# Performance work log

Hardware: AMD Instinct MI355X
Metric: run time of the kernel (lower is better)

Reference implementation:

```python
import jax, jax.numpy as jnp
import numpy as np

B, L, D, H, HD = 4, 4096, 512, 8, 64
BS = 64                 # block_size
NB = L // BS            # num blocks (== max_num_blocks)
MAXNB = 64


def setup_inputs() -> dict:
    key = jax.random.key(0)
    ks = jax.random.split(key, 11)
    s_in = 1.0 / np.sqrt(D)
    s_hd = 1.0 / np.sqrt(HD)
    s_o = 1.0 / np.sqrt(H * HD)
    return {
        "inputs_q": jax.random.normal(ks[0], (B, L, D), jnp.float32),
        "Wq": jax.random.normal(ks[1], (D, H, HD), jnp.float32) * s_in,
        "bq": jnp.zeros((H, HD), jnp.float32),
        "Wk": jax.random.normal(ks[2], (D, H, HD), jnp.float32) * s_in,
        "bk": jnp.zeros((H, HD), jnp.float32),
        "Wv": jax.random.normal(ks[3], (D, H, HD), jnp.float32) * s_in,
        "bv": jnp.zeros((H, HD), jnp.float32),
        "Wsort": jax.random.normal(ks[4], (HD, MAXNB), jnp.float32) * s_hd,
        "bsort": jnp.zeros((MAXNB,), jnp.float32),
        "Wout": jax.random.normal(ks[5], (H, HD, D), jnp.float32) * s_o,
        "bout": jnp.zeros((D,), jnp.float32),
    }


def _block_attention(q, k, v):
    # q,k,v: [b, n_blocks, block, heads, head_dim]; attention within each block
    scale = 1.0 / np.sqrt(HD)
    scores = jnp.einsum("bnqhd,bnkhd->bnhqk", q, k) * scale
    w = jax.nn.softmax(scores, axis=-1)
    return jnp.einsum("bnhqk,bnkhd->bnqhd", w, v)


def reference(inputs_q, Wq, bq, Wk, bk, Wv, bv, Wsort, bsort, Wout, bout):
    # self-attention: inputs_kv = inputs_q; seq_len == blocks_total_len so no padding
    q = jnp.einsum("bld,dhk->blhk", inputs_q, Wq) + bq
    k = jnp.einsum("bld,dhk->blhk", inputs_q, Wk) + bk
    v = jnp.einsum("bld,dhk->blhk", inputs_q, Wv) + bv

    block_q = q.reshape(B, NB, BS, H, HD)
    block_k = k.reshape(B, NB, BS, H, HD)
    block_v = v.reshape(B, NB, BS, H, HD)

    # non-causal: sum keys within each block -> [b, n_kv, h, hd]
    sum_key = jnp.sum(block_k, axis=2)
    sort_out = jnp.einsum("bnhk,ko->bnho", sum_key, Wsort) + bsort
    sort_out = sort_out[:, :, :, :NB]
    permutation = jax.nn.softmax(sort_out, axis=-1)  # [b, n_kv, h, n_q]

    # faithful to original einsum subscripts ('k' and 'l' both contracted)
    sorted_key = jnp.einsum("bkshd,bnhl->bnshd", block_k, permutation)
    sorted_value = jnp.einsum("bkshd,bnhl->bnshd", block_v, permutation)

    x = _block_attention(block_q, block_k, block_v)
    x = x + _block_attention(block_q, sorted_key, sorted_value)

    x = x.reshape(B, L, H, HD)
    out = jnp.einsum("blhd,hdf->blf", x, Wout) + bout
    return out
```

## Files before the change

kernel.cpp:

```cpp
#include <hip/hip_runtime.h>


constexpr int BB   = 4;
constexpr int LL   = 4096;
constexpr int DD   = 512;
constexpr int HH   = 8;
constexpr int HDIM = 64;
constexpr int BS   = 64;
constexpr int NBLK = 64;
constexpr int MTOT = BB * LL;

using f32x4  = __attribute__((ext_vector_type(4))) float;
typedef __attribute__((ext_vector_type(8))) __bf16 bf16x8;

static __device__ __forceinline__ ushort f2bf(float f) {
  uint u = __float_as_uint(f);
  uint r = (u + 0x7fffu + ((u >> 16) & 1u)) >> 16;
  return (ushort)r;
}
static __device__ __forceinline__ float bf2f(ushort u) { return __uint_as_float((uint)u << 16); }
static __device__ __forceinline__ float bflo(uint u) { return __uint_as_float(u << 16); }
static __device__ __forceinline__ float bfhi(uint u) { return __uint_as_float(u & 0xffff0000u); }

static __device__ __forceinline__ int swb(int row, int cb) {
  return (row << 6) + ((cb ^ ((row & 7) << 4)) >> 1);
}

#define GLOBAL_AS(p) ((const __attribute__((address_space(1))) void*)(p))
#define LDS_AS(p)    ((__attribute__((address_space(3))) void*)(p))
#define SB0()        __builtin_amdgcn_sched_barrier(0)

__global__ __launch_bounds__(256) void f32_to_bf16_vec(
    const float* __restrict__ src, ushort* __restrict__ dst)
{
  const int i = blockIdx.x * 256 + threadIdx.x;
  float4 v = reinterpret_cast<const float4*>(src)[i];
  ushort4 o;
  o.x = f2bf(v.x); o.y = f2bf(v.y); o.z = f2bf(v.z); o.w = f2bf(v.w);
  reinterpret_cast<ushort4*>(dst)[i] = o;
}

__global__ __launch_bounds__(256) void transpose_cast4(
    const float* __restrict__ Wq, const float* __restrict__ Wk,
    const float* __restrict__ Wv, const float* __restrict__ Wo,
    ushort* __restrict__ Wqkv_t, ushort* __restrict__ Wout_t)
{
  __shared__ float tile[32][33];
  const int z  = blockIdx.z;
  const float* src = (z == 0) ? Wq : (z == 1) ? Wk : (z == 2) ? Wv : Wo;
  ushort* dst = (z < 3) ? (Wqkv_t + (size_t)z * 512 * 512) : Wout_t;
  const int tx = threadIdx.x & 31, ty = threadIdx.x >> 5;
  const int r0 = blockIdx.y * 32, c0 = blockIdx.x * 32;
  #pragma unroll
  for (int q = 0; q < 4; ++q)
    tile[ty + 8 * q][tx] = src[(size_t)(r0 + ty + 8 * q) * 512 + c0 + tx];
  __syncthreads();
  #pragma unroll
  for (int q = 0; q < 4; ++q)
    dst[(size_t)(c0 + ty + 8 * q) * 512 + r0 + tx] = f2bf(tile[tx][ty + 8 * q]);
}

template<int MODE>
__global__ __launch_bounds__(256, 3) void gemm_pipe3(
    const ushort* __restrict__ A, const ushort* __restrict__ Bt,
    const float* __restrict__ b0, const float* __restrict__ b1,
    const float* __restrict__ b2,
    ushort* __restrict__ Cq, ushort* __restrict__ Ck, ushort* __restrict__ Cv,
    float* __restrict__ Cf, int N, int NBX)
{
  constexpr int K  = 512;
  constexpr int NT = K / 32;
  constexpr int TN = 128;
  __shared__ __align__(16) ushort sA[3][128 * 32];
  __shared__ __align__(16) ushort sB[3][128 * 32];

  const int tid  = threadIdx.x;
  const int lane = tid & 63;
  const int w    = tid >> 6;
  const int wr   = w >> 1, wc = w & 1;
  const int lr   = lane & 15;
  const int kq   = lane >> 4;

  const int nwg  = NBX * 128;
  const int cpx  = nwg >> 3;
  const int swz  = ((int)blockIdx.x & 7) * cpx + ((int)blockIdx.x >> 3);
  const int nb   = swz % NBX;
  const int mb   = swz / NBX;
  const int brow = mb * 128;
  const int bcol = nb * TN;

  auto stageA = [&](int buf, int t, int j) {
    const int c   = j * 256 + tid;
    const int row = c >> 2, ch = c & 3;
    const ushort* src = A + (size_t)(brow + row) * K + t * 32 + ((ch ^ ((row >> 1) & 3)) << 3);
    __builtin_amdgcn_global_load_lds(GLOBAL_AS(src),
        LDS_AS(&sA[buf][(j * 256 + (w << 6)) << 3]), 16, 0, 0);
  };
  auto stageB = [&](int buf, int t, int j) {
    const int c   = j * 256 + tid;
    const int row = c >> 2, ch = c & 3;
    const ushort* src = Bt + (size_t)(bcol + row) * K + t * 32 + ((ch ^ ((row >> 1) & 3)) << 3);
    __builtin_amdgcn_global_load_lds(GLOBAL_AS(src),
        LDS_AS(&sB[buf][(j * 256 + (w << 6)) << 3]), 16, 0, 0);
  };
  auto ldA = [&](int buf, int mf) -> bf16x8 {
    const int row = (wr << 6) + (mf << 4) + lr;
    return *reinterpret_cast<const bf16x8*>(&sA[buf][(row << 5) + ((kq ^ ((row >> 1) & 3)) << 3)]);
  };
  auto ldB = [&](int buf, int nf) -> bf16x8 {
    const int row = (wc << 6) + (nf << 4) + lr;
    return *reinterpret_cast<const bf16x8*>(&sB[buf][(row << 5) + ((kq ^ ((row >> 1) & 3)) << 3)]);
  };

  f32x4 acc[4][4];
  #pragma unroll
  for (int mi = 0; mi < 4; ++mi)
    #pragma unroll
    for (int ni = 0; ni < 4; ++ni)
      acc[mi][ni] = (f32x4){0.f, 0.f, 0.f, 0.f};

  stageA(0, 0, 0); stageA(0, 0, 1); stageB(0, 0, 0); stageB(0, 0, 1);
  stageA(1, 1, 0); stageA(1, 1, 1); stageB(1, 1, 0); stageB(1, 1, 1);
  asm volatile("s_waitcnt vmcnt(4)" ::: "memory");
  SB0(); __builtin_amdgcn_s_barrier(); SB0();

  for (int t = 0; t < NT; ++t) {
    const int buf  = t % 3;
    const int nbuf = (t + 2) % 3;
    const bool more = (t + 2) < NT;

    bf16x8 af[4], bfr[4];
    #pragma unroll
    for (int mf = 0; mf < 4; ++mf) af[mf] = ldA(buf, mf);
    #pragma unroll
    for (int nf = 0; nf < 4; ++nf) bfr[nf] = ldB(buf, nf);
    if (more) { stageA(nbuf, t + 2, 0); stageA(nbuf, t + 2, 1);
                stageB(nbuf, t + 2, 0); stageB(nbuf, t + 2, 1); }
    SB0();
    __builtin_amdgcn_s_setprio(1);
    #pragma unroll
    for (int mi = 0; mi < 4; ++mi)
      #pragma unroll
      for (int ni = 0; ni < 4; ++ni)
        acc[mi][ni] = __builtin_amdgcn_mfma_f32_16x16x32_bf16(af[mi], bfr[ni], acc[mi][ni], 0, 0, 0);
    __builtin_amdgcn_s_setprio(0);
    SB0();
    if (more) asm volatile("s_waitcnt vmcnt(4)" ::: "memory");
    else      asm volatile("s_waitcnt vmcnt(0)" ::: "memory");
    SB0(); __builtin_amdgcn_s_barrier(); SB0();
  }

  if constexpr (MODE == 0) {
    ushort* sEp = (ushort*)&sA[0][0];
    constexpr int ES = TN + 16;
    const int which = bcol >> 9;
    ushort* dst = (which == 0) ? Cq : ((which == 1) ? Ck : Cv);
    const float* bsel = (which == 0) ? b0 : ((which == 1) ? b1 : b2);
    const int ncol0 = bcol & 511;
    #pragma unroll
    for (int mi = 0; mi < 4; ++mi) {
      if (mi) __syncthreads();
      #pragma unroll
      for (int nf = 0; nf < 4; ++nf) {
        const int col = wc * 64 + nf * 16 + lr;
        const float bb = bsel[ncol0 + col];
        #pragma unroll
        for (int r = 0; r < 4; ++r)
          sEp[(wr * 16 + kq * 4 + r) * ES + col] = f2bf(acc[mi][nf][r] + bb);
      }
      __syncthreads();
      #pragma unroll
      for (int it = 0; it < 2; ++it) {
        const int idx = tid + it * 256;
        const int rr  = idx >> 4;
        const int cc  = (idx & 15) * 8;
        uint4 v = *reinterpret_cast<const uint4*>(&sEp[rr * ES + cc]);
        const int grow = brow + (rr >> 4) * 64 + mi * 16 + (rr & 15);
        *reinterpret_cast<uint4*>(&dst[(size_t)grow * DD + ncol0 + cc]) = v;
      }
    }
  } else {
    float* sEpF = (float*)&sA[0][0];
    constexpr int ES = TN + 8;
    #pragma unroll
    for (int mi = 0; mi < 4; ++mi) {
      if (mi) __syncthreads();
      #pragma unroll
      for (int nf = 0; nf < 4; ++nf) {
        const int col = wc * 64 + nf * 16 + lr;
        const float bb = b0[bcol + col];
        #pragma unroll
        for (int r = 0; r < 4; ++r)
          sEpF[(wr * 16 + kq * 4 + r) * ES + col] = acc[mi][nf][r] + bb;
      }
      __syncthreads();
      #pragma unroll
      for (int it = 0; it < 4; ++it) {
        const int idx = tid + it * 256;
        const int rr  = idx >> 5;
        const int cc  = (idx & 31) * 4;
        float4 v = *reinterpret_cast<const float4*>(&sEpF[rr * ES + cc]);
        const int grow = brow + (rr >> 4) * 64 + mi * 16 + (rr & 15);
        *reinterpret_cast<float4*>(&Cf[(size_t)grow * N + bcol + cc]) = v;
      }
    }
  }
}

__global__ __launch_bounds__(256) void sumkv_fused(
    const ushort* __restrict__ K, const ushort* __restrict__ V,
    ushort* __restrict__ Khi, ushort* __restrict__ Klo, ushort* __restrict__ Vb)
{
  __shared__ float kbuf[4][64][9];
  __shared__ float vbuf[4][64][9];
  const int bs   = blockIdx.x;
  const int b    = bs >> 6, s = bs & 63;
  const int lane = threadIdx.x & 63;
  const int kbq  = threadIdx.x >> 6;
  const size_t rowbase = ((size_t)b * LL + s) * DD + lane * 8;

  uint4 ku[16], vu[16];
  #pragma unroll
  for (int i = 0; i < 16; ++i) {
    const size_t off = rowbase + (size_t)(kbq * 16 + i) * BS * DD;
    ku[i] = *reinterpret_cast<const uint4*>(K + off);
    vu[i] = *reinterpret_cast<const uint4*>(V + off);
  }
  float ak[8] = {0,0,0,0,0,0,0,0}, av[8] = {0,0,0,0,0,0,0,0};
  #pragma unroll
  for (int i = 0; i < 16; ++i) {
    ak[0] += bflo(ku[i].x); ak[1] += bfhi(ku[i].x); ak[2] += bflo(ku[i].y); ak[3] += bfhi(ku[i].y);
    ak[4] += bflo(ku[i].z); ak[5] += bfhi(ku[i].z); ak[6] += bflo(ku[i].w); ak[7] += bfhi(ku[i].w);
    av[0] += bflo(vu[i].x); av[1] += bfhi(vu[i].x); av[2] += bflo(vu[i].y); av[3] += bfhi(vu[i].y);
    av[4] += bflo(vu[i].z); av[5] += bfhi(vu[i].z); av[6] += bflo(vu[i].w); av[7] += bfhi(vu[i].w);
  }
  #pragma unroll
  for (int j = 0; j < 8; ++j) { kbuf[kbq][lane][j] = ak[j]; vbuf[kbq][lane][j] = av[j]; }
  __syncthreads();

  const size_t wbase = (size_t)bs * DD + lane * 8;
  if (kbq == 0) {
    uint4 hi4, lo4;
    uint* hp = reinterpret_cast<uint*>(&hi4);
    uint* lp = reinterpret_cast<uint*>(&lo4);
    #pragma unroll
    for (int p = 0; p < 4; ++p) {
      uint hw = 0, lw = 0;
      #pragma unroll
      for (int q = 0; q < 2; ++q) {
        const int j = p * 2 + q;
        const float t = kbuf[0][lane][j] + kbuf[1][lane][j] +
                        kbuf[2][lane][j] + kbuf[3][lane][j];
        const ushort h = f2bf(t);
        const ushort l = f2bf(t - bf2f(h));
        hw |= (uint)h << (16 * q);
        lw |= (uint)l << (16 * q);
      }
      hp[p] = hw; lp[p] = lw;
    }
    *reinterpret_cast<uint4*>(Khi + wbase) = hi4;
    *reinterpret_cast<uint4*>(Klo + wbase) = lo4;
  } else if (kbq == 1) {
    uint4 o4;
    uint* op = reinterpret_cast<uint*>(&o4);
    #pragma unroll
    for (int p = 0; p < 4; ++p) {
      uint wv = 0;
      #pragma unroll
      for (int q = 0; q < 2; ++q) {
        const int j = p * 2 + q;
        const float t = vbuf[0][lane][j] + vbuf[1][lane][j] +
                        vbuf[2][lane][j] + vbuf[3][lane][j];
        wv |= (uint)f2bf(t) << (16 * q);
      }
      op[p] = wv;
    }
    *reinterpret_cast<uint4*>(Vb + wbase) = o4;
  }
}

__global__ __launch_bounds__(256) void attn_mfma(
    const ushort* __restrict__ Q, const ushort* __restrict__ Kg,
    const ushort* __restrict__ Vg, const ushort* __restrict__ Khi,
    const ushort* __restrict__ Klo, const ushort* __restrict__ Vsb,
    ushort* __restrict__ X)
{
  __shared__ __align__(16) ushort sA[64 * 64];
  __shared__ __align__(16) ushort sVt[64 * 64];
  __shared__ __align__(16) ushort sCP[64 * 64];
  const int bid = blockIdx.x;
  const int swz = (bid & 7) * 256 + (bid >> 3);
  const int n = swz & 63, h = (swz >> 6) & 7, b = swz >> 9;
  const int tid  = threadIdx.x;
  const int lane = tid & 63;
  const int w    = tid >> 6;
  const int lr   = lane & 15, hi4 = lane >> 4;
  const float scale = 0.125f;

  const size_t tbase = ((size_t)(b * LL + n * BS)) * DD + h * HDIM;
  const size_t sbase = ((size_t)(b * BS)) * DD + h * HDIM;

  uint4 k1[2], v1[2], k2h[2], k2l[2], v2[2];
  int rr[2], cc[2];
  #pragma unroll
  for (int it = 0; it < 2; ++it) {
    const int i  = tid + it * 256;
    const int r  = i >> 3;
    const int c8 = (i & 7) << 3;
    rr[it] = r; cc[it] = c8;
    const size_t g1 = tbase + (size_t)r * DD + c8;
    const size_t g2 = sbase + (size_t)r * DD + c8;
    k1[it]  = *reinterpret_cast<const uint4*>(Kg  + g1);
    v1[it]  = *reinterpret_cast<const uint4*>(Vg  + g1);
    k2h[it] = *reinterpret_cast<const uint4*>(Khi + g2);
    k2l[it] = *reinterpret_cast<const uint4*>(Klo + g2);
    v2[it]  = *reinterpret_cast<const uint4*>(Vsb + g2);
  }
  bf16x8 qf[2];
  #pragma unroll
  for (int ks = 0; ks < 2; ++ks)
    qf[ks] = *reinterpret_cast<const bf16x8*>(
        Q + tbase + (size_t)(w * 16 + lr) * DD + ks * 32 + hi4 * 8);

  #pragma unroll
  for (int it = 0; it < 2; ++it) {
    *reinterpret_cast<uint4*>(&sA[swb(rr[it], cc[it] << 1)]) = k1[it];
    const uint u[4] = {v1[it].x, v1[it].y, v1[it].z, v1[it].w};
    #pragma unroll
    for (int j = 0; j < 4; ++j) {
      sVt[swb(cc[it] + 2 * j,     rr[it] << 1)] = (ushort)(u[j] & 0xffff);
      sVt[swb(cc[it] + 2 * j + 1, rr[it] << 1)] = (ushort)(u[j] >> 16);
    }
  }
  __syncthreads();

  f32x4 xacc[4];
  #pragma unroll
  for (int dt = 0; dt < 4; ++dt) xacc[dt] = (f32x4){0.f, 0.f, 0.f, 0.f};

  {
    f32x4 st[4];
    #pragma unroll
    for (int t = 0; t < 4; ++t) st[t] = (f32x4){0.f, 0.f, 0.f, 0.f};
    #pragma unroll
    for (int ks = 0; ks < 2; ++ks) {
      #pragma unroll
      for (int t = 0; t < 4; ++t) {
        bf16x8 kf = *reinterpret_cast<const bf16x8*>(
            &sA[swb(t * 16 + lr, (ks * 32 + hi4 * 8) << 1)]);
        st[t] = __builtin_amdgcn_mfma_f32_16x16x32_bf16(kf, qf[ks], st[t], 0, 0, 0);
      }
    }
    float e[4][4];
    float mx = -1e30f;
    #pragma unroll
    for (int t = 0; t < 4; ++t)
      #pragma unroll
      for (int r = 0; r < 4; ++r) { e[t][r] = st[t][r] * scale; mx = fmaxf(mx, e[t][r]); }
    mx = fmaxf(mx, __shfl_xor(mx, 16));
    mx = fmaxf(mx, __shfl_xor(mx, 32));
    float sum = 0.f;
    #pragma unroll
    for (int t = 0; t < 4; ++t)
      #pragma unroll
      for (int r = 0; r < 4; ++r) { e[t][r] = __expf(e[t][r] - mx); sum += e[t][r]; }
    sum += __shfl_xor(sum, 16);
    sum += __shfl_xor(sum, 32);
    const float inv = 1.0f / sum;
    #pragma unroll
    for (int t = 0; t < 4; ++t) {
      ushort4 p4;
      p4.x = f2bf(e[t][0] * inv); p4.y = f2bf(e[t][1] * inv);
      p4.z = f2bf(e[t][2] * inv); p4.w = f2bf(e[t][3] * inv);
      *reinterpret_cast<ushort4*>(&sCP[swb(w * 16 + lr, (t * 16 + hi4 * 4) << 1)]) = p4;
    }
    #pragma unroll
    for (int ks = 0; ks < 2; ++ks) {
      bf16x8 pa = *reinterpret_cast<const bf16x8*>(
          &sCP[swb(w * 16 + lr, (ks * 32 + hi4 * 8) << 1)]);
      #pragma unroll
      for (int dt = 0; dt < 4; ++dt) {
        bf16x8 vb = *reinterpret_cast<const bf16x8*>(
            &sVt[swb(dt * 16 + lr, (ks * 32 + hi4 * 8) << 1)]);
        xacc[dt] = __builtin_amdgcn_mfma_f32_16x16x32_bf16(pa, vb, xacc[dt], 0, 0, 0);
      }
    }
  }
  __syncthreads();

  #pragma unroll
  for (int it = 0; it < 2; ++it) {
    *reinterpret_cast<uint4*>(&sA[swb(rr[it], cc[it] << 1)])  = k2h[it];
    *reinterpret_cast<uint4*>(&sCP[swb(rr[it], cc[it] << 1)]) = k2l[it];
    const uint u[4] = {v2[it].x, v2[it].y, v2[it].z, v2[it].w};
    #pragma unroll
    for (int j = 0; j < 4; ++j) {
      sVt[swb(cc[it] + 2 * j,     rr[it] << 1)] = (ushort)(u[j] & 0xffff);
      sVt[swb(cc[it] + 2 * j + 1, rr[it] << 1)] = (ushort)(u[j] >> 16);
    }
  }
  __syncthreads();

  {
    f32x4 st[4];
    #pragma unroll
    for (int t = 0; t < 4; ++t) st[t] = (f32x4){0.f, 0.f, 0.f, 0.f};
    #pragma unroll
    for (int ks = 0; ks < 2; ++ks) {
      #pragma unroll
      for (int t = 0; t < 4; ++t) {
        bf16x8 kh = *reinterpret_cast<const bf16x8*>(
            &sA[swb(t * 16 + lr, (ks * 32 + hi4 * 8) << 1)]);
        st[t] = __builtin_amdgcn_mfma_f32_16x16x32_bf16(kh, qf[ks], st[t], 0, 0, 0);
        bf16x8 kl = *reinterpret_cast<const bf16x8*>(
            &sCP[swb(t * 16 + lr, (ks * 32 + hi4 * 8) << 1)]);
        st[t] = __builtin_amdgcn_mfma_f32_16x16x32_bf16(kl, qf[ks], st[t], 0, 0, 0);
      }
    }
    __syncthreads();
    float e[4][4];
    float mx = -1e30f;
    #pragma unroll
    for (int t = 0; t < 4; ++t)
      #pragma unroll
      for (int r = 0; r < 4; ++r) { e[t][r] = st[t][r] * scale; mx = fmaxf(mx, e[t][r]); }
    mx = fmaxf(mx, __shfl_xor(mx, 16));
    mx = fmaxf(mx, __shfl_xor(mx, 32));
    float sum = 0.f;
    #pragma unroll
    for (int t = 0; t < 4; ++t)
      #pragma unroll
      for (int r = 0; r < 4; ++r) { e[t][r] = __expf(e[t][r] - mx); sum += e[t][r]; }
    sum += __shfl_xor(sum, 16);
    sum += __shfl_xor(sum, 32);
    const float inv = 1.0f / sum;
    #pragma unroll
    for (int t = 0; t < 4; ++t) {
      ushort4 p4;
      p4.x = f2bf(e[t][0] * inv); p4.y = f2bf(e[t][1] * inv);
      p4.z = f2bf(e[t][2] * inv); p4.w = f2bf(e[t][3] * inv);
      *reinterpret_cast<ushort4*>(&sCP[swb(w * 16 + lr, (t * 16 + hi4 * 4) << 1)]) = p4;
    }
    #pragma unroll
    for (int ks = 0; ks < 2; ++ks) {
      bf16x8 pa = *reinterpret_cast<const bf16x8*>(
          &sCP[swb(w * 16 + lr, (ks * 32 + hi4 * 8) << 1)]);
      #pragma unroll
      for (int dt = 0; dt < 4; ++dt) {
        bf16x8 vb = *reinterpret_cast<const bf16x8*>(
            &sVt[swb(dt * 16 + lr, (ks * 32 + hi4 * 8) << 1)]);
        xacc[dt] = __builtin_amdgcn_mfma_f32_16x16x32_bf16(pa, vb, xacc[dt], 0, 0, 0);
      }
    }
  }

  #pragma unroll
  for (int dt = 0; dt < 4; ++dt)
    #pragma unroll
    for (int r = 0; r < 4; ++r)
      X[tbase + (size_t)(w * 16 + hi4 * 4 + r) * DD + dt * 16 + lr] = f2bf(xacc[dt][r]);
}

extern "C" void kernel_launch(void* const* d_in, const int* in_sizes, int n_in,
                              void* d_out, int out_size, void* d_ws, size_t ws_size,
                              hipStream_t stream) {
  const float* x_in = (const float*)d_in[0];
  const float* Wq   = (const float*)d_in[1];
  const float* bq   = (const float*)d_in[2];
  const float* Wk   = (const float*)d_in[3];
  const float* bk   = (const float*)d_in[4];
  const float* Wv   = (const float*)d_in[5];
  const float* bv   = (const float*)d_in[6];
  const float* Wout = (const float*)d_in[9];
  const float* bout = (const float*)d_in[10];
  float* out = (float*)d_out;

  const size_t NTOK = (size_t)MTOT * DD;
  const size_t NSUM = (size_t)BB * BS * DD;
  char* ws = (char*)d_ws;
  ushort* xb      = (ushort*)ws;            ws += NTOK * 2;
  ushort* Qb      = (ushort*)ws;            ws += NTOK * 2;
  ushort* Kb      = (ushort*)ws;            ws += NTOK * 2;
  ushort* Vb      = (ushort*)ws;            ws += NTOK * 2;
  ushort* Xb      = (ushort*)ws;            ws += NTOK * 2;
  ushort* Wqkv_t  = (ushort*)ws;            ws += (size_t)1536 * 512 * 2;
  ushort* Wout_t  = (ushort*)ws;            ws += (size_t)512 * 512 * 2;
  ushort* KhiB    = (ushort*)ws;            ws += NSUM * 2;
  ushort* KloB    = (ushort*)ws;            ws += NSUM * 2;
  ushort* VsB     = (ushort*)ws;            ws += NSUM * 2;

  f32_to_bf16_vec<<<NTOK / 4 / 256, 256, 0, stream>>>(x_in, xb);
  transpose_cast4<<<dim3(16, 16, 4), 256, 0, stream>>>(
      Wq, Wk, Wv, Wout, Wqkv_t, Wout_t);

  gemm_pipe3<0><<<12 * 128, 256, 0, stream>>>(
      xb, Wqkv_t, bq, bk, bv, Qb, Kb, Vb, nullptr, 1536, 12);

  sumkv_fused<<<BB * BS, 256, 0, stream>>>(Kb, Vb, KhiB, KloB, VsB);

  attn_mfma<<<BB * HH * NBLK, 256, 0, stream>>>(Qb, Kb, Vb, KhiB, KloB, VsB, Xb);

  gemm_pipe3<1><<<4 * 128, 256, 0, stream>>>(
      Xb, Wout_t, bout, nullptr, nullptr, nullptr, nullptr, nullptr, out, 512, 4);
}
```

Before: 99.69 us.

## Replace QKV GEMM with 256x128-tile, 512-thread, double-buffered four-phase kernel

The QKV projection moves from the shared three-stage 128x128 GEMM template to a dedicated kernel with 256x128 tiles, 8 waves, K-steps of 64 and double buffering. Each K-step is split into four barrier-separated MFMA phases, with next-tile global-to-LDS loads issued inside the first two. The larger tile is meant to raise operand reuse and cut the workgroup count. The cost is one workgroup per CU (launch bounds 512,1), more barriers per K-step and bigger LDS use. The output GEMM is split into its own non-templated kernel with unchanged logic.

```diff
diff --git a/kernel.cpp b/kernel.cpp
--- a/kernel.cpp
+++ b/kernel.cpp
@@ -60,17 +60,167 @@
     dst[(size_t)(c0 + ty + 8 * q) * 512 + r0 + tx] = f2bf(tile[tx][ty + 8 * q]);
 }
 
-template<int MODE>
-__global__ __launch_bounds__(256, 3) void gemm_pipe3(
+__global__ __launch_bounds__(512, 1) void qkv_4phase(
     const ushort* __restrict__ A, const ushort* __restrict__ Bt,
     const float* __restrict__ b0, const float* __restrict__ b1,
     const float* __restrict__ b2,
-    ushort* __restrict__ Cq, ushort* __restrict__ Ck, ushort* __restrict__ Cv,
-    float* __restrict__ Cf, int N, int NBX)
+    ushort* __restrict__ Cq, ushort* __restrict__ Ck, ushort* __restrict__ Cv)
+{
+  constexpr int K = 512;
+  __shared__ __align__(16) ushort sA[2][256 * 64];
+  __shared__ __align__(16) ushort sB[2][128 * 64];
+
+  const int tid  = threadIdx.x;
+  const int lane = tid & 63;
+  const int w    = tid >> 6;
+  const int wr   = w >> 1;
+  const int wc   = w & 1;
+  const int lr   = lane & 15;
+  const int kq   = lane >> 4;
+
+  const int cpx  = 768 >> 3;
+  const int swz  = ((int)blockIdx.x & 7) * cpx + ((int)blockIdx.x >> 3);
+  const int nb   = swz % 12;
+  const int mb   = swz / 12;
+  const int brow = mb * 256;
+  const int bcol = nb * 128;
+
+  auto stA = [&](int buf, int kt, int j) {
+    const int c = j * 512 + tid;
+    const int row = c >> 3, g = c & 7;
+    const ushort* src = A + (size_t)(brow + row) * K + kt * 64 + ((g ^ (row & 7)) << 3);
+    __builtin_amdgcn_global_load_lds(GLOBAL_AS(src),
+        LDS_AS(&sA[buf][(j * 512 + w * 64) * 8]), 16, 0, 0);
+  };
+  auto stB = [&](int buf, int kt, int j) {
+    const int c = j * 512 + tid;
+    const int row = c >> 3, g = c & 7;
+    const ushort* src = Bt + (size_t)(bcol + row) * K + kt * 64 + ((g ^ (row & 7)) << 3);
+    __builtin_amdgcn_global_load_lds(GLOBAL_AS(src),
+        LDS_AS(&sB[buf][(j * 512 + w * 64) * 8]), 16, 0, 0);
+  };
+  auto rdA = [&](int buf, int mf, int ks) -> bf16x8 {
+    const int row = wr * 64 + mf * 16 + lr;
+    return *reinterpret_cast<const bf16x8*>(
+        &sA[buf][(row << 6) + ((((ks << 2) + kq) ^ (row & 7)) << 3)]);
+  };
+  auto rdB = [&](int buf, int nf, int ks) -> bf16x8 {
+    const int row = wc * 64 + nf * 16 + lr;
+    return *reinterpret_cast<const bf16x8*>(
+        &sB[buf][(row << 6) + ((((ks << 2) + kq) ^ (row & 7)) << 3)]);
+  };
+
+  f32x4 acc[4][4];
+  #pragma unroll
+  for (int mf = 0; mf < 4; ++mf)
+    #pragma unroll
+    for (int nf = 0; nf < 4; ++nf)
+      acc[mf][nf] = (f32x4){0.f, 0.f, 0.f, 0.f};
+
+  stA(0, 0, 0); stA(0, 0, 1); stA(0, 0, 2); stA(0, 0, 3);
+  stB(0, 0, 0); stB(0, 0, 1);
+  asm volatile("s_waitcnt vmcnt(0)" ::: "memory");
+  SB0(); __builtin_amdgcn_s_barrier(); SB0();
+
+  #pragma unroll 1
+  for (int t = 0; t < 8; ++t) {
+    const int buf  = t & 1;
+    const int nbuf = buf ^ 1;
+    const bool st  = (t + 1) < 8;
+    bf16x8 br[4];
+
+    #pragma unroll
+    for (int nf = 0; nf < 4; ++nf) br[nf] = rdB(buf, nf, 0);
+    {
+      bf16x8 a0 = rdA(buf, 0, 0), a1 = rdA(buf, 1, 0);
+      if (st) { stA(nbuf, t + 1, 0); stA(nbuf, t + 1, 1); stB(nbuf, t + 1, 0); }
+      SB0(); __builtin_amdgcn_s_barrier(); SB0();
+      __builtin_amdgcn_s_setprio(1);
+      #pragma unroll
+      for (int nf = 0; nf < 4; ++nf) {
+        acc[0][nf] = __builtin_amdgcn_mfma_f32_16x16x32_bf16(a0, br[nf], acc[0][nf], 0, 0, 0);
+        acc[1][nf] = __builtin_amdgcn_mfma_f32_16x16x32_bf16(a1, br[nf], acc[1][nf], 0, 0, 0);
+      }
+      __builtin_amdgcn_s_setprio(0);
+    }
+    {
+      bf16x8 a2 = rdA(buf, 2, 0), a3 = rdA(buf, 3, 0);
+      if (st) { stA(nbuf, t + 1, 2); stA(nbuf, t + 1, 3); stB(nbuf, t + 1, 1); }
+      SB0(); __builtin_amdgcn_s_barrier(); SB0();
+      __builtin_amdgcn_s_setprio(1);
+      #pragma unroll
+      for (int nf = 0; nf < 4; ++nf) {
+        acc[2][nf] = __builtin_amdgcn_mfma_f32_16x16x32_bf16(a2, br[nf], acc[2][nf], 0, 0, 0);
+        acc[3][nf] = __builtin_amdgcn_mfma_f32_16x16x32_bf16(a3, br[nf], acc[3][nf], 0, 0, 0);
+      }
+      __builtin_amdgcn_s_setprio(0);
+    }
+    #pragma unroll
+    for (int nf = 0; nf < 4; ++nf) br[nf] = rdB(buf, nf, 1);
+    {
+      bf16x8 a0 = rdA(buf, 0, 1), a1 = rdA(buf, 1, 1);
+      SB0(); __builtin_amdgcn_s_barrier(); SB0();
+      __builtin_amdgcn_s_setprio(1);
+      #pragma unroll
+      for (int nf = 0; nf < 4; ++nf) {
+        acc[0][nf] = __builtin_amdgcn_mfma_f32_16x16x32_bf16(a0, br[nf], acc[0][nf], 0, 0, 0);
+        acc[1][nf] = __builtin_amdgcn_mfma_f32_16x16x32_bf16(a1, br[nf], acc[1][nf], 0, 0, 0);
+      }
+      __builtin_amdgcn_s_setprio(0);
+    }
+    {
+      bf16x8 a2 = rdA(buf, 2, 1), a3 = rdA(buf, 3, 1);
+      SB0(); __builtin_amdgcn_s_barrier(); SB0();
+      __builtin_amdgcn_s_setprio(1);
+      #pragma unroll
+      for (int nf = 0; nf < 4; ++nf) {
+        acc[2][nf] = __builtin_amdgcn_mfma_f32_16x16x32_bf16(a2, br[nf], acc[2][nf], 0, 0, 0);
+        acc[3][nf] = __builtin_amdgcn_mfma_f32_16x16x32_bf16(a3, br[nf], acc[3][nf], 0, 0, 0);
+      }
+      __builtin_amdgcn_s_setprio(0);
+      SB0();
+      if (st) asm volatile("s_waitcnt vmcnt(0)" ::: "memory");
+      SB0(); __builtin_amdgcn_s_barrier(); SB0();
+    }
+  }
+
+  ushort* sEp = (ushort*)&sA[0][0];
+  constexpr int ES = 128 + 16;
+  const int which = bcol >> 9;
+  ushort* dst = (which == 0) ? Cq : ((which == 1) ? Ck : Cv);
+  const float* bsel = (which == 0) ? b0 : ((which == 1) ? b1 : b2);
+  const int ncol0 = bcol & 511;
+  #pragma unroll
+  for (int mf = 0; mf < 4; ++mf) {
+    if (mf) __syncthreads();
+    #pragma unroll
+    for (int nf = 0; nf < 4; ++nf) {
+      const int col = wc * 64 + nf * 16 + lr;
+      const float bb = bsel[ncol0 + col];
+      #pragma unroll
+      for (int r = 0; r < 4; ++r)
+        sEp[(wr * 16 + kq * 4 + r) * ES + col] = f2bf(acc[mf][nf][r] + bb);
+    }
+    __syncthreads();
+    #pragma unroll
+    for (int it = 0; it < 2; ++it) {
+      const int idx = tid + it * 512;
+      const int rr  = idx >> 4;
+      const int cc  = (idx & 15) * 8;
+      uint4 v = *reinterpret_cast<const uint4*>(&sEp[rr * ES + cc]);
+      const int grow = brow + (rr >> 4) * 64 + mf * 16 + (rr & 15);
+      *reinterpret_cast<uint4*>(&dst[(size_t)grow * DD + ncol0 + cc]) = v;
+    }
+  }
+}
+
+__global__ __launch_bounds__(256, 3) void gemm_out(
+    const ushort* __restrict__ A, const ushort* __restrict__ Bt,
+    const float* __restrict__ bias, float* __restrict__ Cf)
 {
   constexpr int K  = 512;
   constexpr int NT = K / 32;
-  constexpr int TN = 128;
+  constexpr int N  = 512;
   __shared__ __align__(16) ushort sA[3][128 * 32];
   __shared__ __align__(16) ushort sB[3][128 * 32];
 
@@ -81,13 +231,12 @@
   const int lr   = lane & 15;
   const int kq   = lane >> 4;
 
-  const int nwg  = NBX * 128;
-  const int cpx  = nwg >> 3;
+  const int cpx  = 512 >> 3;
   const int swz  = ((int)blockIdx.x & 7) * cpx + ((int)blockIdx.x >> 3);
-  const int nb   = swz % NBX;
-  const int mb   = swz / NBX;
+  const int nb   = swz % 4;
+  const int mb   = swz / 4;
   const int brow = mb * 128;
-  const int bcol = nb * TN;
+  const int bcol = nb * 128;
 
   auto stageA = [&](int buf, int t, int j) {
     const int c   = j * 256 + tid;
@@ -150,59 +299,28 @@
     SB0(); __builtin_amdgcn_s_barrier(); SB0();
   }
 
-  if constexpr (MODE == 0) {
-    ushort* sEp = (ushort*)&sA[0][0];
-    constexpr int ES = TN + 16;
-    const int which = bcol >> 9;
-    ushort* dst = (which == 0) ? Cq : ((which == 1) ? Ck : Cv);
-    const float* bsel = (which == 0) ? b0 : ((which == 1) ? b1 : b2);
-    const int ncol0 = bcol & 511;
-    #pragma unroll
-    for (int mi = 0; mi < 4; ++mi) {
-      if (mi) __syncthreads();
-      #pragma unroll
-      for (int nf = 0; nf < 4; ++nf) {
-        const int col = wc * 64 + nf * 16 + lr;
-        const float bb = bsel[ncol0 + col];
-        #pragma unroll
-        for (int r = 0; r < 4; ++r)
-          sEp[(wr * 16 + kq * 4 + r) * ES + col] = f2bf(acc[mi][nf][r] + bb);
-      }
-      __syncthreads();
-      #pragma unroll
-      for (int it = 0; it < 2; ++it) {
-        const int idx = tid + it * 256;
-        const int rr  = idx >> 4;
-        const int cc  = (idx & 15) * 8;
-        uint4 v = *reinterpret_cast<const uint4*>(&sEp[rr * ES + cc]);
-        const int grow = brow + (rr >> 4) * 64 + mi * 16 + (rr & 15);
-        *reinterpret_cast<uint4*>(&dst[(size_t)grow * DD + ncol0 + cc]) = v;
-      }
-    }
-  } else {
-    float* sEpF = (float*)&sA[0][0];
-    constexpr int ES = TN + 8;
-    #pragma unroll
-    for (int mi = 0; mi < 4; ++mi) {
-      if (mi) __syncthreads();
-      #pragma unroll
-      for (int nf = 0; nf < 4; ++nf) {
-        const int col = wc * 64 + nf * 16 + lr;
-        const float bb = b0[bcol + col];
-        #pragma unroll
-        for (int r = 0; r < 4; ++r)
-          sEpF[(wr * 16 + kq * 4 + r) * ES + col] = acc[mi][nf][r] + bb;
-      }
-      __syncthreads();
-      #pragma unroll
-      for (int it = 0; it < 4; ++it) {
-        const int idx = tid + it * 256;
-        const int rr  = idx >> 5;
-        const int cc  = (idx & 31) * 4;
-        float4 v = *reinterpret_cast<const float4*>(&sEpF[rr * ES + cc]);
-        const int grow = brow + (rr >> 4) * 64 + mi * 16 + (rr & 15);
-        *reinterpret_cast<float4*>(&Cf[(size_t)grow * N + bcol + cc]) = v;
-      }
+  float* sEpF = (float*)&sA[0][0];
+  constexpr int ES = 128 + 8;
+  #pragma unroll
+  for (int mi = 0; mi < 4; ++mi) {
+    if (mi) __syncthreads();
+    #pragma unroll
+    for (int nf = 0; nf < 4; ++nf) {
+      const int col = wc * 64 + nf * 16 + lr;
+      const float bb = bias[bcol + col];
+      #pragma unroll
+      for (int r = 0; r < 4; ++r)
+        sEpF[(wr * 16 + kq * 4 + r) * ES + col] = acc[mi][nf][r] + bb;
+    }
+    __syncthreads();
+    #pragma unroll
+    for (int it = 0; it < 4; ++it) {
+      const int idx = tid + it * 256;
+      const int rr  = idx >> 5;
+      const int cc  = (idx & 31) * 4;
+      float4 v = *reinterpret_cast<const float4*>(&sEpF[rr * ES + cc]);
+      const int grow = brow + (rr >> 4) * 64 + mi * 16 + (rr & 15);
+      *reinterpret_cast<float4*>(&Cf[(size_t)grow * N + bcol + cc]) = v;
     }
   }
 }
@@ -493,13 +611,12 @@
   transpose_cast4<<<dim3(16, 16, 4), 256, 0, stream>>>(
       Wq, Wk, Wv, Wout, Wqkv_t, Wout_t);
 
-  gemm_pipe3<0><<<12 * 128, 256, 0, stream>>>(
-      xb, Wqkv_t, bq, bk, bv, Qb, Kb, Vb, nullptr, 1536, 12);
+  qkv_4phase<<<768, 512, 0, stream>>>(
+      xb, Wqkv_t, bq, bk, bv, Qb, Kb, Vb);
 
   sumkv_fused<<<BB * BS, 256, 0, stream>>>(Kb, Vb, KhiB, KloB, VsB);
 
   attn_mfma<<<BB * HH * NBLK, 256, 0, stream>>>(Qb, Kb, Vb, KhiB, KloB, VsB, Xb);
 
-  gemm_pipe3<1><<<4 * 128, 256, 0, stream>>>(
-      Xb, Wout_t, bout, nullptr, nullptr, nullptr, nullptr, nullptr, out, 512, 4);
-}
+  gemm_out<<<4 * 128, 256, 0, stream>>>(Xb, Wout_t, bout, out);
+}
```

New measurement: 107.8 us. 1.08x slower.
